# Kernel optimization log

Hardware: AMD Instinct MI355X
Metric: run time of the kernel (lower is better)

Reference implementation:

```python
import jax, jax.numpy as jnp
import numpy as np

N = 256        # ImageSize
NC = 8         # coils
NSPOKE = 34    # radial spokes
NVEC = 512     # samples per spoke
K = NSPOKE * NVEC  # total k-space points


def setup_inputs() -> dict:
    key = jax.random.key(0)
    k1, k2, k3, k4 = jax.random.split(key, 4)
    input_r = jax.random.normal(k1, (N, N, 2), dtype=jnp.float32)
    C_r = jax.random.normal(k2, (NC, N, N, 2), dtype=jnp.float32)
    w = jax.random.uniform(k3, (NVEC,), dtype=jnp.float32)
    # nonuniform k-space coordinates in [-pi, pi)
    angle = jax.random.uniform(k4, (K, 2), dtype=jnp.float32,
                               minval=-np.pi, maxval=np.pi)
    return {"input_r": input_r, "C_r": C_r, "w": w, "angle": angle}


def reference(input_r, C_r, w, angle):
    # Type-3 NUFFT: y[c,k] = sum_j C[c,j]*x[j] * exp(-i*(s_k*(-x1_j) + t_k*(-x2_j)))
    #             = sum_{a,b} (C[c,a,b]*x[a,b]) * exp(+i*s_k*g[a]) * exp(+i*t_k*g[b])
    # since the source grid is separable: x1_j = g[a], x2_j = g[b],
    # g = linspace(-N//2, N//2-1, N) for even N (iflag=0 -> negative sign).
    n = input_r.shape[0]
    nvec = w.shape[0]
    g = jnp.arange(n, dtype=jnp.float32) - n // 2          # [N]

    x = input_r[..., 0] + 1j * input_r[..., 1]             # [N,N] complex64
    C = C_r[..., 0] + 1j * C_r[..., 1]                     # [Nc,N,N] complex64
    Xc = C * x[None]                                       # coil-weighted image [Nc,N,N]

    s = angle[:, 0]                                        # [K]
    t = angle[:, 1]                                        # [K]
    E1 = jnp.exp(1j * s[:, None] * g[None, :])             # [K,N] phase along axis a
    E2 = jnp.exp(1j * t[:, None] * g[None, :])             # [K,N] phase along axis b

    # contract b first -> [Nc,K,N], then a -> [Nc,K]
    y = jnp.einsum('kb,cab,ka->ck', E2, Xc, E1, optimize=True)  # [Nc,K]

    # density compensation: wr = tile(w, (Nc, Nspoke, 1)).reshape(Nc, -1)
    wr = jnp.tile(w, y.shape[1] // nvec)                   # [K]
    y = y * wr[None, :]

    return jnp.stack([jnp.real(y), jnp.imag(y)], axis=-1)  # [Nc,K,2] float32
```

## Files before the change

### kernel.cpp

```cpp
#include <hip/hip_runtime.h>
#include <hip/hip_bf16.h>
#include <stdint.h>


#define NKTOT 17408
#define NBLK 272
#define NT 8

typedef short bf16x8 __attribute__((ext_vector_type(8)));
typedef float f32x4 __attribute__((ext_vector_type(4)));

__device__ __forceinline__ unsigned short f2bf(float f) {
  unsigned int u = __builtin_bit_cast(unsigned int, f);
  u += 0x7FFFu + ((u >> 16) & 1u);
  return (unsigned short)(u >> 16);
}
__device__ __forceinline__ unsigned int pk2bf(float lo, float hi) {
  return (unsigned int)f2bf(lo) | ((unsigned int)f2bf(hi) << 16);
}

__device__ __forceinline__ size_t aidx(int c, int m, int jj) {
  int tt = jj >> 5;
  int s = ((m & 1) << 2) | ((jj >> 3) & 3);
  return (((size_t)(c * 8 + tt) * 256 + (m >> 1)) * 8 + s) * 8 + (jj & 7);
}

__global__ __launch_bounds__(256) void pack_a(
    const float* __restrict__ input_r, const float* __restrict__ C_r,
    unsigned short* __restrict__ Apack, float* __restrict__ biastab)
{
  const int bx = blockIdx.x;
  const int tid = threadIdx.x;
  const int p = bx * 2 + (tid >> 7);
  const int a = p & 255;
  const int c = p >> 8;
  const int j = tid & 127;
  const size_t xbase = (size_t)a * 256;
  const size_t cbase = ((size_t)(c * 256 + a)) * 256;
  if (j == 0) {
    float xr = input_r[(xbase + 128) * 2], xi = input_r[(xbase + 128) * 2 + 1];
    float cr = C_r[(cbase + 128) * 2],     ci = C_r[(cbase + 128) * 2 + 1];
    biastab[c * 512 + a]       = cr * xr - ci * xi;
    biastab[c * 512 + 256 + a] = cr * xi + ci * xr;
    xr = input_r[xbase * 2]; xi = input_r[xbase * 2 + 1];
    cr = C_r[cbase * 2];     ci = C_r[cbase * 2 + 1];
    float reb = cr * xr - ci * xi, imb = cr * xi + ci * xr;
    Apack[aidx(c, a, 127)]       = f2bf(reb);
    Apack[aidx(c, a, 255)]       = f2bf(imb);
    Apack[aidx(c, 256 + a, 127)] = f2bf(imb);
    Apack[aidx(c, 256 + a, 255)] = f2bf(-reb);
  } else {
    const int bp = 128 + j, bm = 128 - j;
    float xpr = input_r[(xbase + bp) * 2], xpi = input_r[(xbase + bp) * 2 + 1];
    float cpr = C_r[(cbase + bp) * 2],     cpi = C_r[(cbase + bp) * 2 + 1];
    float pr = cpr * xpr - cpi * xpi, pi = cpr * xpi + cpi * xpr;
    float xmr = input_r[(xbase + bm) * 2], xmi = input_r[(xbase + bm) * 2 + 1];
    float cmr = C_r[(cbase + bm) * 2],     cmi = C_r[(cbase + bm) * 2 + 1];
    float mrv = cmr * xmr - cmi * xmi, miv = cmr * xmi + cmi * xmr;
    Apack[aidx(c, a, j - 1)]         = f2bf(pr + mrv);
    Apack[aidx(c, a, 127 + j)]       = f2bf(miv - pi);
    Apack[aidx(c, 256 + a, j - 1)]   = f2bf(pi + miv);
    Apack[aidx(c, 256 + a, 127 + j)] = f2bf(pr - mrv);
  }
}

__device__ __forceinline__ void b_compute(unsigned short* buf, float2 et,
                                          float t, int tile, int w, int l,
                                          int bwoff) {
  const float jb = (float)((tile & 3) * 32 + w * 4 + 1);
  float s0, c0;
  __sincosf(t * jb, &s0, &c0);
  float c1 = c0 * et.x - s0 * et.y, s1 = s0 * et.x + c0 * et.y;
  float c2 = c1 * et.x - s1 * et.y, s2 = s1 * et.x + c1 * et.y;
  float c3 = c2 * et.x - s2 * et.y, s3 = s2 * et.x + c2 * et.y;
  const bool use_cos = tile < 4;
  float v0 = use_cos ? c0 : s0;
  float v1 = use_cos ? c1 : s1;
  float v2 = use_cos ? c2 : s2;
  float v3 = use_cos ? c3 : s3;
  uint2 pk;
  pk.x = pk2bf(v0, v1);
  pk.y = pk2bf(v2, v3);
  *(uint2*)(buf + bwoff) = pk;
}

__global__ __launch_bounds__(512, 4) void gemm_fused(
    const unsigned short* __restrict__ Apack,
    const float* __restrict__ biastab,
    const float* __restrict__ angle,
    const float* __restrict__ wvec,
    float* __restrict__ out)
{
  __shared__ unsigned short Bs[8][2048];
  __shared__ float scol[8][2][64];

  const int bx = blockIdx.x;
  const int c = (bx >> 3) & 7;
  const int ktile = (bx >> 6) * 8 + (bx & 7);
  const int kt0 = ktile * 64;
  const int tid = threadIdx.x;
  const int w = tid >> 6;
  const int l = tid & 63;
  const int lhi = l >> 4;
  const int llo = l & 15;

  const unsigned short* Alane = Apack + (size_t)c * (8 * 16384)
      + (size_t)(w * 32 + (llo >> 1)) * 64 + (((llo & 1) << 2) | lhi) * 8;
  const float* biasp = biastab + c * 512 + w * 64 + lhi * 4;

  const int u8 = ((((llo & 1) << 2) | lhi) ^ ((llo >> 1) & 7)) * 8;
  const int plbase = llo >> 1;

  const float t_reg = angle[(size_t)(kt0 + l) * 2 + 1];
  float2 et;
  __sincosf(t_reg, &et.y, &et.x);
  const int bwoff = (l >> 1) * 64 +
      ((((l & 1) << 2) | (w >> 1)) ^ ((l >> 1) & 7)) * 8 + (w & 1) * 4;

  f32x4 acc[4][4];
#pragma unroll
  for (int fi = 0; fi < 4; ++fi) {
    f32x4 b4 = *(const f32x4*)(biasp + fi * 16);
#pragma unroll
    for (int fj = 0; fj < 4; ++fj) acc[fi][fj] = b4;
  }

#pragma unroll
  for (int tt = 0; tt < NT; ++tt)
    b_compute(&Bs[tt][0], et, t_reg, tt, w, l, bwoff);
  __syncthreads();

#pragma unroll 2
  for (int tt = 0; tt < NT; ++tt) {
    bf16x8 af[4];
#pragma unroll
    for (int fi = 0; fi < 4; ++fi)
      af[fi] = *(const bf16x8*)(Alane + (size_t)tt * 16384 + fi * 512);
    bf16x8 bfr[4];
#pragma unroll
    for (int fj = 0; fj < 4; ++fj)
      bfr[fj] = *(const bf16x8*)&Bs[tt][(fj * 8 + plbase) * 64 + u8];
#pragma unroll
    for (int fi = 0; fi < 4; ++fi)
#pragma unroll
      for (int fj = 0; fj < 4; ++fj)
        acc[fi][fj] = __builtin_amdgcn_mfma_f32_16x16x32_bf16(
            af[fi], bfr[fj], acc[fi][fj], 0, 0, 0);
  }

  const int aoff = (w & 3) * 64;
  const float a0f = (float)(aoff + lhi * 4 - 128);
#pragma unroll
  for (int fj = 0; fj < 4; ++fj) {
    const int col = fj * 16 + llo;
    const int k = kt0 + col;
    const float s = angle[(size_t)k * 2];
    float s1, c1, sY, cY;
    __sincosf(s, &s1, &c1);
    __sincosf(16.f * s, &sY, &cY);
    float c2 = c1 * c1 - s1 * s1, s2 = 2.f * c1 * s1;
    float c3 = c2 * c1 - s2 * s1, s3 = c2 * s1 + s2 * c1;
    float cY2 = cY * cY - sY * sY, sY2 = 2.f * cY * sY;
    float cY3 = cY2 * cY - sY2 * sY, sY3 = cY2 * sY + sY2 * cY;
    const float Yr[4] = {1.f, cY, cY2, cY3};
    const float Yi[4] = {0.f, sY, sY2, sY3};
    float Or = 0.f, Oi = 0.f;
#pragma unroll
    for (int fi = 0; fi < 4; ++fi) {
      float v0 = acc[fi][fj][0], v1 = acc[fi][fj][1];
      float v2 = acc[fi][fj][2], v3 = acc[fi][fj][3];
      float Ir = v0 + c1 * v1 + c2 * v2 + c3 * v3;
      float Ii = s1 * v1 + s2 * v2 + s3 * v3;
      Or += Yr[fi] * Ir - Yi[fi] * Ii;
      Oi += Yi[fi] * Ir + Yr[fi] * Ii;
    }
    float sb, cb;
    __sincosf(s * a0f, &sb, &cb);
    float sumr = cb * Or - sb * Oi;
    float sumi = sb * Or + cb * Oi;
    sumr += __shfl_xor(sumr, 16, 64);
    sumr += __shfl_xor(sumr, 32, 64);
    sumi += __shfl_xor(sumi, 16, 64);
    sumi += __shfl_xor(sumi, 32, 64);
    if (lhi == 0) {
      scol[w][0][col] = sumr;
      scol[w][1][col] = sumi;
    }
  }
  __syncthreads();
  if (tid < 128) {
    const int col = tid >> 1;
    const int comp = tid & 1;
    const int k = kt0 + col;
    float re = scol[0][0][col] + scol[1][0][col] + scol[2][0][col] + scol[3][0][col]
             - scol[4][1][col] - scol[5][1][col] - scol[6][1][col] - scol[7][1][col];
    float im = scol[0][1][col] + scol[1][1][col] + scol[2][1][col] + scol[3][1][col]
             + scol[4][0][col] + scol[5][0][col] + scol[6][0][col] + scol[7][0][col];
    float val = comp ? im : re;
    out[((size_t)c * NKTOT + k) * 2 + comp] = val * wvec[k & 511];
  }
}

extern "C" void kernel_launch(void* const* d_in, const int* in_sizes, int n_in,
                              void* d_out, int out_size, void* d_ws, size_t ws_size,
                              hipStream_t stream) {
  const float* input_r = (const float*)d_in[0];
  const float* C_r     = (const float*)d_in[1];
  const float* wvec    = (const float*)d_in[2];
  const float* angle   = (const float*)d_in[3];
  float* out = (float*)d_out;

  unsigned short* Apack = (unsigned short*)d_ws;
  float* biastab = (float*)((char*)d_ws + (size_t)2097152);

  pack_a<<<1024, 256, 0, stream>>>(input_r, C_r, Apack, biastab);
  gemm_fused<<<8 * NBLK, 512, 0, stream>>>(Apack, biastab, angle, wvec, out);
}
```

Before: 113.1 us.

## Switch fused GEMM to 32x32x16 MFMA with new A/B layouts

Replaces the 16x16x32 bf16 MFMA tiling with 32x32x16 MFMAs on 2x2 accumulator blocks. It repacks A in global memory and B in shared memory (XOR-swizzled chunks) to match the new operand layout. B generation now uses a rotating phasor recurrence of 32 steps per thread, not one sincos per group of four. The epilogue is reorganised around the 32-row layout, which needs one fewer shuffle stage. The aims are fewer MFMA issues, fewer operand loads and less sincos work. The trade-offs are higher register pressure and more phase error from the longer recurrence.

```diff
diff --git a/kernel.cpp b/kernel.cpp
--- a/kernel.cpp
+++ b/kernel.cpp
@@ -9,6 +9,7 @@
 
 typedef short bf16x8 __attribute__((ext_vector_type(8)));
 typedef float f32x4 __attribute__((ext_vector_type(4)));
+typedef float f32x16 __attribute__((ext_vector_type(16)));
 
 __device__ __forceinline__ unsigned short f2bf(float f) {
   unsigned int u = __builtin_bit_cast(unsigned int, f);
@@ -20,9 +21,8 @@
 }
 
 __device__ __forceinline__ size_t aidx(int c, int m, int jj) {
-  int tt = jj >> 5;
-  int s = ((m & 1) << 2) | ((jj >> 3) & 3);
-  return (((size_t)(c * 8 + tt) * 256 + (m >> 1)) * 8 + s) * 8 + (jj & 7);
+  int tt = jj >> 5, q = (jj >> 4) & 1, h = (jj >> 3) & 1;
+  return (size_t)c * 131072 + (tt * 2 + q) * 8192 + h * 4096 + m * 8 + (jj & 7);
 }
 
 __global__ __launch_bounds__(256) void pack_a(
@@ -64,26 +64,6 @@
   }
 }
 
-__device__ __forceinline__ void b_compute(unsigned short* buf, float2 et,
-                                          float t, int tile, int w, int l,
-                                          int bwoff) {
-  const float jb = (float)((tile & 3) * 32 + w * 4 + 1);
-  float s0, c0;
-  __sincosf(t * jb, &s0, &c0);
-  float c1 = c0 * et.x - s0 * et.y, s1 = s0 * et.x + c0 * et.y;
-  float c2 = c1 * et.x - s1 * et.y, s2 = s1 * et.x + c1 * et.y;
-  float c3 = c2 * et.x - s2 * et.y, s3 = s2 * et.x + c2 * et.y;
-  const bool use_cos = tile < 4;
-  float v0 = use_cos ? c0 : s0;
-  float v1 = use_cos ? c1 : s1;
-  float v2 = use_cos ? c2 : s2;
-  float v3 = use_cos ? c3 : s3;
-  uint2 pk;
-  pk.x = pk2bf(v0, v1);
-  pk.y = pk2bf(v2, v3);
-  *(uint2*)(buf + bwoff) = pk;
-}
-
 __global__ __launch_bounds__(512, 4) void gemm_fused(
     const unsigned short* __restrict__ Apack,
     const float* __restrict__ biastab,
@@ -91,7 +71,7 @@
     const float* __restrict__ wvec,
     float* __restrict__ out)
 {
-  __shared__ unsigned short Bs[8][2048];
+  __shared__ unsigned short Bs[64 * 256];
   __shared__ float scol[8][2][64];
 
   const int bx = blockIdx.x;
@@ -101,88 +81,110 @@
   const int tid = threadIdx.x;
   const int w = tid >> 6;
   const int l = tid & 63;
-  const int lhi = l >> 4;
-  const int llo = l & 15;
-
-  const unsigned short* Alane = Apack + (size_t)c * (8 * 16384)
-      + (size_t)(w * 32 + (llo >> 1)) * 64 + (((llo & 1) << 2) | lhi) * 8;
-  const float* biasp = biastab + c * 512 + w * 64 + lhi * 4;
-
-  const int u8 = ((((llo & 1) << 2) | lhi) ^ ((llo >> 1) & 7)) * 8;
-  const int plbase = llo >> 1;
-
-  const float t_reg = angle[(size_t)(kt0 + l) * 2 + 1];
-  float2 et;
-  __sincosf(t_reg, &et.y, &et.x);
-  const int bwoff = (l >> 1) * 64 +
-      ((((l & 1) << 2) | (w >> 1)) ^ ((l >> 1) & 7)) * 8 + (w & 1) * 4;
-
-  f32x4 acc[4][4];
-#pragma unroll
-  for (int fi = 0; fi < 4; ++fi) {
-    f32x4 b4 = *(const f32x4*)(biasp + fi * 16);
-#pragma unroll
-    for (int fj = 0; fj < 4; ++fj) acc[fi][fj] = b4;
-  }
-
-#pragma unroll
-  for (int tt = 0; tt < NT; ++tt)
-    b_compute(&Bs[tt][0], et, t_reg, tt, w, l, bwoff);
+  const int l31 = l & 31;
+  const int l5 = l >> 5;
+
+  const unsigned short* Alane = Apack + (size_t)c * 131072
+      + l5 * 4096 + (size_t)(w * 64 + l31) * 8;
+
+  {
+    const float t_reg = angle[(size_t)(kt0 + l) * 2 + 1];
+    float2 et;
+    __sincosf(t_reg, &et.y, &et.x);
+    float zr, zi;
+    __sincosf(t_reg * (float)((w & 3) * 32 + 1), &zi, &zr);
+    const bool use_cos = (w < 4);
+#pragma unroll
+    for (int oc = 0; oc < 4; ++oc) {
+      float v[8];
+#pragma unroll
+      for (int o8 = 0; o8 < 8; ++o8) {
+        v[o8] = use_cos ? zr : zi;
+        float nr = zr * et.x - zi * et.y;
+        float ni = zr * et.y + zi * et.x;
+        zr = nr; zi = ni;
+      }
+      uint4 pk;
+      pk.x = pk2bf(v[0], v[1]);
+      pk.y = pk2bf(v[2], v[3]);
+      pk.z = pk2bf(v[4], v[5]);
+      pk.w = pk2bf(v[6], v[7]);
+      const int chunk = w * 4 + oc;
+      const int pos = (chunk & 24) | ((chunk & 7) ^ (l & 7));
+      *(uint4*)&Bs[l * 256 + pos * 8] = pk;
+    }
+  }
+
+  f32x16 acc[2][2];
+#pragma unroll
+  for (int rg = 0; rg < 2; ++rg) {
+#pragma unroll
+    for (int q2 = 0; q2 < 4; ++q2) {
+      f32x4 b4 = *(const f32x4*)(biastab + c * 512 + w * 64 + rg * 32
+                                 + 4 * l5 + 8 * q2);
+#pragma unroll
+      for (int r2 = 0; r2 < 4; ++r2) {
+        acc[rg][0][q2 * 4 + r2] = b4[r2];
+        acc[rg][1][q2 * 4 + r2] = b4[r2];
+      }
+    }
+  }
   __syncthreads();
 
 #pragma unroll 2
   for (int tt = 0; tt < NT; ++tt) {
-    bf16x8 af[4];
-#pragma unroll
-    for (int fi = 0; fi < 4; ++fi)
-      af[fi] = *(const bf16x8*)(Alane + (size_t)tt * 16384 + fi * 512);
-    bf16x8 bfr[4];
-#pragma unroll
-    for (int fj = 0; fj < 4; ++fj)
-      bfr[fj] = *(const bf16x8*)&Bs[tt][(fj * 8 + plbase) * 64 + u8];
-#pragma unroll
-    for (int fi = 0; fi < 4; ++fi)
-#pragma unroll
-      for (int fj = 0; fj < 4; ++fj)
-        acc[fi][fj] = __builtin_amdgcn_mfma_f32_16x16x32_bf16(
-            af[fi], bfr[fj], acc[fi][fj], 0, 0, 0);
-  }
-
-  const int aoff = (w & 3) * 64;
-  const float a0f = (float)(aoff + lhi * 4 - 128);
-#pragma unroll
-  for (int fj = 0; fj < 4; ++fj) {
-    const int col = fj * 16 + llo;
+#pragma unroll
+    for (int q = 0; q < 2; ++q) {
+      const int ks = tt * 2 + q;
+      bf16x8 af0 = *(const bf16x8*)(Alane + (size_t)ks * 8192);
+      bf16x8 af1 = *(const bf16x8*)(Alane + (size_t)ks * 8192 + 256);
+      const int chunk = ks * 2 + l5;
+      const int pos8 = ((chunk & 24) | ((chunk & 7) ^ (l & 7))) * 8;
+      bf16x8 bf0 = *(const bf16x8*)&Bs[l31 * 256 + pos8];
+      bf16x8 bf1 = *(const bf16x8*)&Bs[(32 + l31) * 256 + pos8];
+      acc[0][0] = __builtin_amdgcn_mfma_f32_32x32x16_bf16(af0, bf0, acc[0][0], 0, 0, 0);
+      acc[0][1] = __builtin_amdgcn_mfma_f32_32x32x16_bf16(af0, bf1, acc[0][1], 0, 0, 0);
+      acc[1][0] = __builtin_amdgcn_mfma_f32_32x32x16_bf16(af1, bf0, acc[1][0], 0, 0, 0);
+      acc[1][1] = __builtin_amdgcn_mfma_f32_32x32x16_bf16(af1, bf1, acc[1][1], 0, 0, 0);
+    }
+  }
+
+#pragma unroll
+  for (int cg = 0; cg < 2; ++cg) {
+    const int col = cg * 32 + l31;
     const int k = kt0 + col;
     const float s = angle[(size_t)k * 2];
-    float s1, c1, sY, cY;
+    float s1, c1, s8, c8;
     __sincosf(s, &s1, &c1);
-    __sincosf(16.f * s, &sY, &cY);
+    __sincosf(8.f * s, &s8, &c8);
     float c2 = c1 * c1 - s1 * s1, s2 = 2.f * c1 * s1;
     float c3 = c2 * c1 - s2 * s1, s3 = c2 * s1 + s2 * c1;
-    float cY2 = cY * cY - sY * sY, sY2 = 2.f * cY * sY;
-    float cY3 = cY2 * cY - sY2 * sY, sY3 = cY2 * sY + sY2 * cY;
-    const float Yr[4] = {1.f, cY, cY2, cY3};
-    const float Yi[4] = {0.f, sY, sY2, sY3};
-    float Or = 0.f, Oi = 0.f;
-#pragma unroll
-    for (int fi = 0; fi < 4; ++fi) {
-      float v0 = acc[fi][fj][0], v1 = acc[fi][fj][1];
-      float v2 = acc[fi][fj][2], v3 = acc[fi][fj][3];
-      float Ir = v0 + c1 * v1 + c2 * v2 + c3 * v3;
-      float Ii = s1 * v1 + s2 * v2 + s3 * v3;
-      Or += Yr[fi] * Ir - Yi[fi] * Ii;
-      Oi += Yi[fi] * Ir + Yr[fi] * Ii;
-    }
-    float sb, cb;
-    __sincosf(s * a0f, &sb, &cb);
-    float sumr = cb * Or - sb * Oi;
-    float sumi = sb * Or + cb * Oi;
-    sumr += __shfl_xor(sumr, 16, 64);
+    float c16 = c8 * c8 - s8 * s8, s16 = 2.f * c8 * s8;
+    float c24 = c16 * c8 - s16 * s8, s24 = s16 * c8 + c16 * s8;
+    const float Yr[4] = {1.f, c8, c16, c24};
+    const float Yi[4] = {0.f, s8, s16, s24};
+    float sumr = 0.f, sumi = 0.f;
+#pragma unroll
+    for (int rg = 0; rg < 2; ++rg) {
+      float Or = 0.f, Oi = 0.f;
+#pragma unroll
+      for (int q2 = 0; q2 < 4; ++q2) {
+        float v0 = acc[rg][cg][q2 * 4 + 0], v1 = acc[rg][cg][q2 * 4 + 1];
+        float v2 = acc[rg][cg][q2 * 4 + 2], v3 = acc[rg][cg][q2 * 4 + 3];
+        float Ir = v0 + c1 * v1 + c2 * v2 + c3 * v3;
+        float Ii = s1 * v1 + s2 * v2 + s3 * v3;
+        Or += Yr[q2] * Ir - Yi[q2] * Ii;
+        Oi += Yi[q2] * Ir + Yr[q2] * Ii;
+      }
+      const float a0f = (float)((w & 3) * 64 + rg * 32 + 4 * l5 - 128);
+      float sb, cb;
+      __sincosf(s * a0f, &sb, &cb);
+      sumr += cb * Or - sb * Oi;
+      sumi += sb * Or + cb * Oi;
+    }
     sumr += __shfl_xor(sumr, 32, 64);
-    sumi += __shfl_xor(sumi, 16, 64);
     sumi += __shfl_xor(sumi, 32, 64);
-    if (lhi == 0) {
+    if (l5 == 0) {
       scol[w][0][col] = sumr;
       scol[w][1][col] = sumi;
     }
```

After: 114.0 us. Within noise of the previous version (+0.7%).
